# Kernel optimization log

Measured on AMD Instinct MI355X. Metric: run time of the kernel, lower is better.

## Reference

```python
import jax, jax.numpy as jnp
import numpy as np

N_HEAD = 16
D_HEAD = 64


def setup_inputs() -> dict:
    key = jax.random.key(0)
    k1, k2, k3 = jax.random.split(key, 3)
    B, L, D = 2, 2048, 1024
    inp = jax.random.normal(k1, (B, L, D), dtype=jnp.float32)
    # causal mask: True -> masked (matches torch masked_fill_ semantics)
    mask = jnp.triu(jnp.ones((L, L), dtype=bool), k=1)[None, None, :, :]
    W_qkv = jax.random.normal(k2, (D, 3 * N_HEAD * D_HEAD), dtype=jnp.float32) * 0.02
    b_qkv = jnp.zeros((3 * N_HEAD * D_HEAD,), dtype=jnp.float32)
    W_out = jax.random.normal(k3, (N_HEAD * D_HEAD, D), dtype=jnp.float32) * 0.02
    b_out = jnp.zeros((D,), dtype=jnp.float32)
    return {"input": inp, "mask": mask, "W_qkv": W_qkv, "b_qkv": b_qkv,
            "W_out": W_out, "b_out": b_out}


def reference(input, mask, W_qkv, b_qkv, W_out, b_out):
    B, L, D = input.shape
    qkv = input @ W_qkv + b_qkv                       # [B, L, 3*H*Dh]
    q, k, v = jnp.split(qkv, 3, axis=-1)              # each [B, L, H*Dh]
    qh = q.reshape(B, L, N_HEAD, D_HEAD)
    kh = k.reshape(B, L, N_HEAD, D_HEAD)
    vh = v.reshape(B, L, N_HEAD, D_HEAD)
    scale = 1.0 / (D_HEAD ** 0.5)
    attn = jnp.einsum('bqhd,bkhd->bhqk', qh, kh) * scale  # [B, H, L, L]
    attn = jnp.where(mask, -jnp.inf, attn)
    attn = jax.nn.softmax(attn, axis=-1)
    out = jnp.einsum('bhqk,bkhd->bqhd', attn, vh).reshape(B, L, D)
    out = out @ W_out + b_out
    # next_memory equivalent: (k, v) pre-head-split, as in the torch code
    return (out, k, v)
```

## Files before the change

kernel.cpp:

```cpp
#include <hip/hip_runtime.h>
#include <cstdint>

#define NHEAD 16
#define DHEAD 64
#define SEQ   2048
#define DMODEL 1024
#define MTOT  4096
#define NQKV  3072

typedef __bf16 bf16x8 __attribute__((ext_vector_type(8)));
typedef short  s16x4  __attribute__((ext_vector_type(4)));
typedef float  f32x4  __attribute__((ext_vector_type(4)));

__device__ __forceinline__ unsigned short f2bf(float f) {
  union { float f; unsigned u; } v; v.f = f;
  unsigned r = v.u + 0x7fffu + ((v.u >> 16) & 1u);
  return (unsigned short)(r >> 16);
}

__device__ __forceinline__ void gl_lds16(const void* g, void* l) {
  __builtin_amdgcn_global_load_lds(
      reinterpret_cast<const __attribute__((address_space(1))) unsigned int*>(
          reinterpret_cast<uintptr_t>(g)),
      reinterpret_cast<__attribute__((address_space(3))) unsigned int*>(
          reinterpret_cast<uintptr_t>(l)),
      16, 0, 0);
}

#if __has_builtin(__builtin_amdgcn_mfma_f32_16x16x16bf16_1k)
#define MFMA_PV(a, b, c) __builtin_amdgcn_mfma_f32_16x16x16bf16_1k(a, b, c, 0, 0, 0)
#else
__device__ __forceinline__ f32x4 mfma_pv_asm(s16x4 a, s16x4 b, f32x4 c) {
  f32x4 d;
  asm volatile("v_mfma_f32_16x16x16_bf16 %0, %1, %2, %3"
               : "=v"(d) : "v"(a), "v"(b), "v"(c));
  return d;
}
#define MFMA_PV(a, b, c) mfma_pv_asm(a, b, c)
#endif

__global__ void k_cvt_bf16(const float* __restrict__ x,
                           unsigned short* __restrict__ y, int n4) {
  int i = blockIdx.x * blockDim.x + threadIdx.x;
  if (i >= n4) return;
  float4 v = reinterpret_cast<const float4*>(x)[i];
  ushort4 o;
  o.x = f2bf(v.x); o.y = f2bf(v.y); o.z = f2bf(v.z); o.w = f2bf(v.w);
  reinterpret_cast<ushort4*>(y)[i] = o;
}

__global__ void k_transpose_cvt2(const float* __restrict__ W0, unsigned short* __restrict__ T0,
                                 const float* __restrict__ W1, unsigned short* __restrict__ T1) {
  __shared__ unsigned short t[32][33];
  const int bx = blockIdx.x;
  const float* W = (bx < 96) ? W0 : W1;
  unsigned short* WT = (bx < 96) ? T0 : T1;
  const int N = (bx < 96) ? 3072 : 1024;
  const int n0 = ((bx < 96) ? bx : (bx - 96)) * 32;
  const int k0 = blockIdx.y * 32;
  const int tx = threadIdx.x, ty = threadIdx.y;
  for (int i = ty; i < 32; i += 8)
    t[i][tx] = f2bf(W[(size_t)(k0 + i) * N + n0 + tx]);
  __syncthreads();
  for (int i = ty; i < 32; i += 8)
    WT[(size_t)(n0 + i) * 1024 + k0 + tx] = t[tx][i];
}

__global__ void k_vtrans(const unsigned short* __restrict__ v,
                         unsigned short* __restrict__ vt) {
  __shared__ unsigned short t[32][33];
  const int bh = blockIdx.z;
  const int t0 = blockIdx.x * 32, d0 = blockIdx.y * 32;
  const int tx = threadIdx.x, ty = threadIdx.y;
  const unsigned short* vb = v + (size_t)bh * SEQ * DHEAD;
  unsigned short* vtb = vt + (size_t)bh * DHEAD * SEQ;
  for (int i = ty; i < 32; i += 8)
    t[i][tx] = vb[(size_t)(t0 + i) * DHEAD + d0 + tx];
  __syncthreads();
  for (int i = ty; i < 32; i += 8)
    vtb[(size_t)(d0 + i) * SEQ + t0 + tx] = t[tx][i];
}

__global__ __launch_bounds__(256, 3) void k_gemm_qkv(
    const unsigned short* __restrict__ A, const unsigned short* __restrict__ Bt,
    const float* __restrict__ bias, float* __restrict__ outbase,
    unsigned short* __restrict__ qbf, unsigned short* __restrict__ kbf,
    unsigned short* __restrict__ vbf) {
  __shared__ __attribute__((aligned(16))) unsigned short As[128 * 64];
  __shared__ __attribute__((aligned(16))) unsigned short Bs[128 * 64];
  const int tid = threadIdx.x, lane = tid & 63;
  const int w = tid >> 6, wm = w >> 1, wn = w & 1;
  const int c = lane & 15, q = lane >> 4, cx = c & 7;
  const int bm = blockIdx.x * 128, bn = blockIdx.y * 128;
  const int srow = tid >> 3, swz8 = ((tid & 7) ^ (srow & 7)) * 8;
  const unsigned short* Ag = A + (size_t)(bm + srow) * DMODEL + swz8;
  const unsigned short* Bg = Bt + (size_t)(bn + srow) * DMODEL + swz8;
  f32x4 acc[4][4] = {};

  for (int kt = 0; kt < DMODEL / 64; ++kt) {
    if (kt) __syncthreads();
    const int k0 = kt * 64;
#pragma unroll
    for (int is = 0; is < 4; ++is) {
      gl_lds16(Ag + k0 + is * 32 * DMODEL, As + is * 2048 + tid * 8);
      gl_lds16(Bg + k0 + is * 32 * DMODEL, Bs + is * 2048 + tid * 8);
    }
    __syncthreads();
#pragma unroll
    for (int k32 = 0; k32 < 2; ++k32) {
      const int ch = ((k32 << 2) | q) ^ cx;
      bf16x8 af[4], bfr[4];
#pragma unroll
      for (int i = 0; i < 4; ++i)
        af[i] = *reinterpret_cast<const bf16x8*>(As + (wm * 64 + i * 16 + c) * 64 + ch * 8);
#pragma unroll
      for (int j = 0; j < 4; ++j)
        bfr[j] = *reinterpret_cast<const bf16x8*>(Bs + (wn * 64 + j * 16 + c) * 64 + ch * 8);
#pragma unroll
      for (int i = 0; i < 4; ++i)
#pragma unroll
        for (int j = 0; j < 4; ++j)
          acc[i][j] = __builtin_amdgcn_mfma_f32_16x16x32_bf16(af[i], bfr[j], acc[i][j], 0, 0, 0);
    }
  }

  const int sec = bn >> 10;
#pragma unroll
  for (int j = 0; j < 4; ++j) {
    const int gn = bn + wn * 64 + j * 16 + c;
    const float bv = bias[gn];
    const int cc = gn & 1023, hh = cc >> 6, dd = cc & 63;
#pragma unroll
    for (int i = 0; i < 4; ++i) {
#pragma unroll
      for (int r = 0; r < 4; ++r) {
        const int gm = bm + wm * 64 + i * 16 + q * 4 + r;
        const int bb = gm >> 11, tok = gm & 2047;
        const float val = acc[i][j][r] + bv;
        const size_t hoff = ((size_t)(bb * NHEAD + hh) * SEQ + tok) * DHEAD + dd;
        if (sec == 0) {
          qbf[hoff] = f2bf(val);
        } else if (sec == 1) {
          outbase[(size_t)4194304 + (size_t)gm * DMODEL + cc] = val;
          kbf[hoff] = f2bf(val);
        } else {
          outbase[(size_t)8388608 + (size_t)gm * DMODEL + cc] = val;
          vbf[hoff] = f2bf(val);
        }
      }
    }
  }
}

__global__ __launch_bounds__(256) void k_attn(
    const unsigned short* __restrict__ qbf, const unsigned short* __restrict__ kbf,
    const unsigned short* __restrict__ vtbf, unsigned short* __restrict__ aout) {
  __shared__ __attribute__((aligned(16))) unsigned short Ks[128 * 64];
  __shared__ __attribute__((aligned(16))) unsigned short Vs[64 * 128];

  const int tid = threadIdx.x, lane = tid & 63, w = tid >> 6;
  const int c = lane & 15, q = lane >> 4;
  const int oo = blockIdx.x >> 5, kk = oo & 7, ssl = oo >> 3;
  const int qsub = (ssl == 0) ? (31 - kk) : (ssl == 1) ? kk
                 : (ssl == 2) ? (23 - kk) : (8 + kk);
  const int bh = blockIdx.x & 31;
  const int kmax = qsub >> 1;
  const size_t hoff = (size_t)bh * SEQ * DHEAD;

  const unsigned short* qg = qbf + hoff + (size_t)(qsub * 64 + w * 16 + c) * DHEAD;
  const bf16x8 qb0 = *reinterpret_cast<const bf16x8*>(qg + q * 8);
  const bf16x8 qb1 = *reinterpret_cast<const bf16x8*>(qg + 32 + q * 8);

  f32x4 o[4] = {};
  float mrun = -__builtin_inff(), lrun = 0.f;
  const float sscale = 0.125f * 1.44269504088896340736f;
  const int qloc = (qsub & 1) * 64 + w * 16 + c;
  const int cx = c & 7;

  const int krow = tid >> 3, kswz = (tid & 7) ^ (krow & 7);
  const int vrow = tid >> 4, vswz = (tid & 15) ^ (vrow & 7);
  const unsigned short* kgb = kbf + hoff;
  const unsigned short* vgb = vtbf + (size_t)bh * DHEAD * SEQ;

  for (int kt = 0; kt <= kmax; ++kt) {
    __syncthreads();
    const unsigned short* kg = kgb + (size_t)kt * 128 * DHEAD;
#pragma unroll
    for (int is = 0; is < 4; ++is)
      gl_lds16(kg + (krow + is * 32) * 64 + kswz * 8, Ks + is * 2048 + tid * 8);
    const unsigned short* vg = vgb + kt * 128;
#pragma unroll
    for (int is = 0; is < 4; ++is)
      gl_lds16(vg + (size_t)(vrow + is * 16) * SEQ + vswz * 8, Vs + is * 2048 + tid * 8);
    __syncthreads();

    f32x4 s[8];
#pragma unroll
    for (int mi = 0; mi < 8; ++mi) {
      const unsigned short* kr = Ks + (mi * 16 + c) * 64;
      const bf16x8 ak0 = *reinterpret_cast<const bf16x8*>(kr + (q ^ cx) * 8);
      const bf16x8 ak1 = *reinterpret_cast<const bf16x8*>(kr + ((4 + q) ^ cx) * 8);
      f32x4 t = {};
      t = __builtin_amdgcn_mfma_f32_16x16x32_bf16(ak0, qb0, t, 0, 0, 0);
      t = __builtin_amdgcn_mfma_f32_16x16x32_bf16(ak1, qb1, t, 0, 0, 0);
      s[mi] = t;
    }

    if (kt == kmax) {
#pragma unroll
      for (int mi = 0; mi < 8; ++mi)
#pragma unroll
        for (int r = 0; r < 4; ++r)
          if (mi * 16 + q * 4 + r > qloc) s[mi][r] = -__builtin_inff();
    }

    float mx = -__builtin_inff();
#pragma unroll
    for (int mi = 0; mi < 8; ++mi)
#pragma unroll
      for (int r = 0; r < 4; ++r) mx = fmaxf(mx, s[mi][r]);
    mx = fmaxf(mx, __shfl_xor(mx, 16));
    mx = fmaxf(mx, __shfl_xor(mx, 32));
    const float mn = fmaxf(mrun, mx * sscale);
    const float al = __builtin_amdgcn_exp2f(mrun - mn);
    mrun = mn;

    float rs = 0.f;
    s16x4 pb[8];
#pragma unroll
    for (int mi = 0; mi < 8; ++mi) {
      const float p0 = __builtin_amdgcn_exp2f(__builtin_fmaf(s[mi][0], sscale, -mn));
      const float p1 = __builtin_amdgcn_exp2f(__builtin_fmaf(s[mi][1], sscale, -mn));
      const float p2 = __builtin_amdgcn_exp2f(__builtin_fmaf(s[mi][2], sscale, -mn));
      const float p3 = __builtin_amdgcn_exp2f(__builtin_fmaf(s[mi][3], sscale, -mn));
      rs += (p0 + p1) + (p2 + p3);
      union { s16x4 v; unsigned u[2]; } pk;
      pk.u[0] = __builtin_amdgcn_perm(__float_as_uint(p1), __float_as_uint(p0), 0x07060302u);
      pk.u[1] = __builtin_amdgcn_perm(__float_as_uint(p3), __float_as_uint(p2), 0x07060302u);
      pb[mi] = pk.v;
    }
    rs += __shfl_xor(rs, 16);
    rs += __shfl_xor(rs, 32);
    lrun = lrun * al + rs;
#pragma unroll
    for (int dm = 0; dm < 4; ++dm) o[dm] *= al;

#pragma unroll
    for (int dm = 0; dm < 4; ++dm) {
      const unsigned short* vr = Vs + (dm * 16 + c) * 128 + (q & 1) * 4;
#pragma unroll
      for (int kf = 0; kf < 8; ++kf) {
        const s16x4 av = *reinterpret_cast<const s16x4*>(
            vr + (((kf * 2 + (q >> 1)) ^ cx) * 8));
        o[dm] = MFMA_PV(av, pb[kf], o[dm]);
      }
    }
  }

  const float linv = 1.0f / lrun;
  const int b = bh >> 4, h = bh & 15;
  const int row = b * SEQ + qsub * 64 + w * 16 + c;
#pragma unroll
  for (int dm = 0; dm < 4; ++dm) {
    ushort4 ov;
    ov.x = f2bf(o[dm][0] * linv);
    ov.y = f2bf(o[dm][1] * linv);
    ov.z = f2bf(o[dm][2] * linv);
    ov.w = f2bf(o[dm][3] * linv);
    *reinterpret_cast<ushort4*>(aout + (size_t)row * DMODEL + h * 64 + dm * 16 + q * 4) = ov;
  }
}

__global__ __launch_bounds__(256) void k_gemm_out(
    const unsigned short* __restrict__ A, const unsigned short* __restrict__ Bt,
    const float* __restrict__ bias, float* __restrict__ C) {
  __shared__ __attribute__((aligned(16))) unsigned short As[128 * 64];
  __shared__ __attribute__((aligned(16))) unsigned short Bs[64 * 64];
  const int tid = threadIdx.x, lane = tid & 63;
  const int w = tid >> 6, wm = w >> 1, wn = w & 1;
  const int c = lane & 15, q = lane >> 4, cx = c & 7;
  const int bm = blockIdx.x * 128, bn = blockIdx.y * 64;
  const int srow = tid >> 3, swz8 = ((tid & 7) ^ (srow & 7)) * 8;
  const unsigned short* Ag = A + (size_t)(bm + srow) * DMODEL + swz8;
  const unsigned short* Bg = Bt + (size_t)(bn + srow) * DMODEL + swz8;
  f32x4 acc[4][2] = {};

  for (int kt = 0; kt < DMODEL / 64; ++kt) {
    if (kt) __syncthreads();
    const int k0 = kt * 64;
#pragma unroll
    for (int is = 0; is < 4; ++is)
      gl_lds16(Ag + k0 + is * 32 * DMODEL, As + is * 2048 + tid * 8);
#pragma unroll
    for (int is = 0; is < 2; ++is)
      gl_lds16(Bg + k0 + is * 32 * DMODEL, Bs + is * 2048 + tid * 8);
    __syncthreads();
#pragma unroll
    for (int k32 = 0; k32 < 2; ++k32) {
      const int ch = ((k32 << 2) | q) ^ cx;
      bf16x8 af[4], bfr[2];
#pragma unroll
      for (int i = 0; i < 4; ++i)
        af[i] = *reinterpret_cast<const bf16x8*>(As + (wm * 64 + i * 16 + c) * 64 + ch * 8);
#pragma unroll
      for (int j = 0; j < 2; ++j)
        bfr[j] = *reinterpret_cast<const bf16x8*>(Bs + (wn * 32 + j * 16 + c) * 64 + ch * 8);
#pragma unroll
      for (int i = 0; i < 4; ++i)
#pragma unroll
        for (int j = 0; j < 2; ++j)
          acc[i][j] = __builtin_amdgcn_mfma_f32_16x16x32_bf16(af[i], bfr[j], acc[i][j], 0, 0, 0);
    }
  }

#pragma unroll
  for (int j = 0; j < 2; ++j) {
    const int gn = bn + wn * 32 + j * 16 + c;
    const float bv = bias[gn];
#pragma unroll
    for (int i = 0; i < 4; ++i)
#pragma unroll
      for (int r = 0; r < 4; ++r) {
        const int gm = bm + wm * 64 + i * 16 + q * 4 + r;
        C[(size_t)gm * DMODEL + gn] = acc[i][j][r] + bv;
      }
  }
}

extern "C" void kernel_launch(void* const* d_in, const int* in_sizes, int n_in,
                              void* d_out, int out_size, void* d_ws, size_t ws_size,
                              hipStream_t stream) {
  (void)in_sizes; (void)n_in; (void)out_size; (void)ws_size;
  const float* input = (const float*)d_in[0];
  const float* W_qkv = (const float*)d_in[2];
  const float* b_qkv = (const float*)d_in[3];
  const float* W_out = (const float*)d_in[4];
  const float* b_out = (const float*)d_in[5];
  float* out = (float*)d_out;

  unsigned char* ws = (unsigned char*)d_ws;
  unsigned short* Abf   = (unsigned short*)(ws + 0);
  unsigned short* VTbf  = (unsigned short*)(ws + 0);
  unsigned short* WqkvT = (unsigned short*)(ws + 8388608);
  unsigned short* WoutT = (unsigned short*)(ws + 14680064);
  unsigned short* Qbf   = (unsigned short*)(ws + 16777216);
  unsigned short* Kbf   = (unsigned short*)(ws + 25165824);
  unsigned short* Vbf   = (unsigned short*)(ws + 33554432);
  unsigned short* Aout  = (unsigned short*)(ws + 41943040);

  k_cvt_bf16<<<4096, 256, 0, stream>>>(input, Abf, 1048576);
  k_transpose_cvt2<<<dim3(128, 32), dim3(32, 8), 0, stream>>>(W_qkv, WqkvT, W_out, WoutT);
  k_gemm_qkv<<<dim3(32, 24), 256, 0, stream>>>(Abf, WqkvT, b_qkv, out, Qbf, Kbf, Vbf);
  k_vtrans<<<dim3(64, 2, 32), dim3(32, 8), 0, stream>>>(Vbf, VTbf);
  k_attn<<<1024, 256, 0, stream>>>(Qbf, Kbf, VTbf, Aout);
  k_gemm_out<<<dim3(32, 16), 256, 0, stream>>>(Aout, WoutT, b_out, out);
}
```

Baseline: 204.0 us.

## Double-buffer LDS tiles with BK=32 in QKV and output projection GEMMs

Both projection GEMMs move from a single-buffered BK=64 LDS tile to two BK=32 buffers. The next tile's global-to-LDS loads are issued before computing on the current one, leaving one barrier per iteration. The intent is to hide global load latency behind MFMA work. The LDS swizzle is redone for the 32-wide rows, and the number of K iterations doubles, which doubles the barriers. There is also a possible race: the prefetch into the other buffer may not be complete when the next iteration's barrier is reached, since the async LDS load has no explicit wait.

```diff
diff --git a/kernel.cpp b/kernel.cpp
--- a/kernel.cpp
+++ b/kernel.cpp
@@ -86,42 +86,48 @@
     const float* __restrict__ bias, float* __restrict__ outbase,
     unsigned short* __restrict__ qbf, unsigned short* __restrict__ kbf,
     unsigned short* __restrict__ vbf) {
-  __shared__ __attribute__((aligned(16))) unsigned short As[128 * 64];
-  __shared__ __attribute__((aligned(16))) unsigned short Bs[128 * 64];
+  __shared__ __attribute__((aligned(16))) unsigned short As[2][128 * 32];
+  __shared__ __attribute__((aligned(16))) unsigned short Bs[2][128 * 32];
   const int tid = threadIdx.x, lane = tid & 63;
   const int w = tid >> 6, wm = w >> 1, wn = w & 1;
-  const int c = lane & 15, q = lane >> 4, cx = c & 7;
+  const int c = lane & 15, q = lane >> 4;
+  const int kc = (c & 3) ^ ((c >> 2) & 3);
   const int bm = blockIdx.x * 128, bn = blockIdx.y * 128;
-  const int srow = tid >> 3, swz8 = ((tid & 7) ^ (srow & 7)) * 8;
-  const unsigned short* Ag = A + (size_t)(bm + srow) * DMODEL + swz8;
-  const unsigned short* Bg = Bt + (size_t)(bn + srow) * DMODEL + swz8;
+  const int srow = tid >> 2;
+  const int skey = (srow & 3) ^ ((srow >> 2) & 3);
+  const int scolsw = (((tid & 3) ^ skey) << 3);
+  const unsigned short* Ag = A + (size_t)(bm + srow) * DMODEL + scolsw;
+  const unsigned short* Bg = Bt + (size_t)(bn + srow) * DMODEL + scolsw;
   f32x4 acc[4][4] = {};
 
-  for (int kt = 0; kt < DMODEL / 64; ++kt) {
-    if (kt) __syncthreads();
-    const int k0 = kt * 64;
-#pragma unroll
-    for (int is = 0; is < 4; ++is) {
-      gl_lds16(Ag + k0 + is * 32 * DMODEL, As + is * 2048 + tid * 8);
-      gl_lds16(Bg + k0 + is * 32 * DMODEL, Bs + is * 2048 + tid * 8);
-    }
+  gl_lds16(Ag, As[0] + tid * 8);
+  gl_lds16(Ag + (size_t)64 * DMODEL, As[0] + 2048 + tid * 8);
+  gl_lds16(Bg, Bs[0] + tid * 8);
+  gl_lds16(Bg + (size_t)64 * DMODEL, Bs[0] + 2048 + tid * 8);
+
+  for (int kt = 0; kt < 32; ++kt) {
+    const int cur = kt & 1;
     __syncthreads();
-#pragma unroll
-    for (int k32 = 0; k32 < 2; ++k32) {
-      const int ch = ((k32 << 2) | q) ^ cx;
-      bf16x8 af[4], bfr[4];
-#pragma unroll
-      for (int i = 0; i < 4; ++i)
-        af[i] = *reinterpret_cast<const bf16x8*>(As + (wm * 64 + i * 16 + c) * 64 + ch * 8);
+    if (kt < 31) {
+      const int k0 = (kt + 1) * 32;
+      gl_lds16(Ag + k0, As[cur ^ 1] + tid * 8);
+      gl_lds16(Ag + k0 + (size_t)64 * DMODEL, As[cur ^ 1] + 2048 + tid * 8);
+      gl_lds16(Bg + k0, Bs[cur ^ 1] + tid * 8);
+      gl_lds16(Bg + k0 + (size_t)64 * DMODEL, Bs[cur ^ 1] + 2048 + tid * 8);
+    }
+    const int ch = (q ^ kc) << 3;
+    bf16x8 af[4], bfr[4];
+#pragma unroll
+    for (int i = 0; i < 4; ++i)
+      af[i] = *reinterpret_cast<const bf16x8*>(As[cur] + (wm * 64 + i * 16 + c) * 32 + ch);
+#pragma unroll
+    for (int j = 0; j < 4; ++j)
+      bfr[j] = *reinterpret_cast<const bf16x8*>(Bs[cur] + (wn * 64 + j * 16 + c) * 32 + ch);
+#pragma unroll
+    for (int i = 0; i < 4; ++i)
 #pragma unroll
       for (int j = 0; j < 4; ++j)
-        bfr[j] = *reinterpret_cast<const bf16x8*>(Bs + (wn * 64 + j * 16 + c) * 64 + ch * 8);
-#pragma unroll
-      for (int i = 0; i < 4; ++i)
-#pragma unroll
-        for (int j = 0; j < 4; ++j)
-          acc[i][j] = __builtin_amdgcn_mfma_f32_16x16x32_bf16(af[i], bfr[j], acc[i][j], 0, 0, 0);
-    }
+        acc[i][j] = __builtin_amdgcn_mfma_f32_16x16x32_bf16(af[i], bfr[j], acc[i][j], 0, 0, 0);
   }
 
   const int sec = bn >> 10;
@@ -274,43 +280,46 @@
 __global__ __launch_bounds__(256) void k_gemm_out(
     const unsigned short* __restrict__ A, const unsigned short* __restrict__ Bt,
     const float* __restrict__ bias, float* __restrict__ C) {
-  __shared__ __attribute__((aligned(16))) unsigned short As[128 * 64];
-  __shared__ __attribute__((aligned(16))) unsigned short Bs[64 * 64];
+  __shared__ __attribute__((aligned(16))) unsigned short As[2][128 * 32];
+  __shared__ __attribute__((aligned(16))) unsigned short Bs[2][64 * 32];
   const int tid = threadIdx.x, lane = tid & 63;
   const int w = tid >> 6, wm = w >> 1, wn = w & 1;
-  const int c = lane & 15, q = lane >> 4, cx = c & 7;
+  const int c = lane & 15, q = lane >> 4;
+  const int kc = (c & 3) ^ ((c >> 2) & 3);
   const int bm = blockIdx.x * 128, bn = blockIdx.y * 64;
-  const int srow = tid >> 3, swz8 = ((tid & 7) ^ (srow & 7)) * 8;
-  const unsigned short* Ag = A + (size_t)(bm + srow) * DMODEL + swz8;
-  const unsigned short* Bg = Bt + (size_t)(bn + srow) * DMODEL + swz8;
+  const int srow = tid >> 2;
+  const int skey = (srow & 3) ^ ((srow >> 2) & 3);
+  const int scolsw = (((tid & 3) ^ skey) << 3);
+  const unsigned short* Ag = A + (size_t)(bm + srow) * DMODEL + scolsw;
+  const unsigned short* Bg = Bt + (size_t)(bn + srow) * DMODEL + scolsw;
   f32x4 acc[4][2] = {};
 
-  for (int kt = 0; kt < DMODEL / 64; ++kt) {
-    if (kt) __syncthreads();
-    const int k0 = kt * 64;
-#pragma unroll
-    for (int is = 0; is < 4; ++is)
-      gl_lds16(Ag + k0 + is * 32 * DMODEL, As + is * 2048 + tid * 8);
-#pragma unroll
-    for (int is = 0; is < 2; ++is)
-      gl_lds16(Bg + k0 + is * 32 * DMODEL, Bs + is * 2048 + tid * 8);
+  gl_lds16(Ag, As[0] + tid * 8);
+  gl_lds16(Ag + (size_t)64 * DMODEL, As[0] + 2048 + tid * 8);
+  gl_lds16(Bg, Bs[0] + tid * 8);
+
+  for (int kt = 0; kt < 32; ++kt) {
+    const int cur = kt & 1;
     __syncthreads();
-#pragma unroll
-    for (int k32 = 0; k32 < 2; ++k32) {
-      const int ch = ((k32 << 2) | q) ^ cx;
-      bf16x8 af[4], bfr[2];
-#pragma unroll
-      for (int i = 0; i < 4; ++i)
-        af[i] = *reinterpret_cast<const bf16x8*>(As + (wm * 64 + i * 16 + c) * 64 + ch * 8);
+    if (kt < 31) {
+      const int k0 = (kt + 1) * 32;
+      gl_lds16(Ag + k0, As[cur ^ 1] + tid * 8);
+      gl_lds16(Ag + k0 + (size_t)64 * DMODEL, As[cur ^ 1] + 2048 + tid * 8);
+      gl_lds16(Bg + k0, Bs[cur ^ 1] + tid * 8);
+    }
+    const int ch = (q ^ kc) << 3;
+    bf16x8 af[4], bfr[2];
+#pragma unroll
+    for (int i = 0; i < 4; ++i)
+      af[i] = *reinterpret_cast<const bf16x8*>(As[cur] + (wm * 64 + i * 16 + c) * 32 + ch);
+#pragma unroll
+    for (int j = 0; j < 2; ++j)
+      bfr[j] = *reinterpret_cast<const bf16x8*>(Bs[cur] + (wn * 32 + j * 16 + c) * 32 + ch);
+#pragma unroll
+    for (int i = 0; i < 4; ++i)
 #pragma unroll
       for (int j = 0; j < 2; ++j)
-        bfr[j] = *reinterpret_cast<const bf16x8*>(Bs + (wn * 32 + j * 16 + c) * 64 + ch * 8);
-#pragma unroll
-      for (int i = 0; i < 4; ++i)
-#pragma unroll
-        for (int j = 0; j < 2; ++j)
-          acc[i][j] = __builtin_amdgcn_mfma_f32_16x16x32_bf16(af[i], bfr[j], acc[i][j], 0, 0, 0);
-    }
+        acc[i][j] = __builtin_amdgcn_mfma_f32_16x16x32_bf16(af[i], bfr[j], acc[i][j], 0, 0, 0);
   }
 
 #pragma unroll
```

After: 201.7 us. About the same (-1.2%).
